# Kernel tuning notes

Measured on AMD Instinct MI355X. Metric: run time of the kernel, lower is better.

Reference implementation:

```python
import jax, jax.numpy as jnp
import numpy as np

MAX_NUM_CENTERS = 100
CENTER_IGNORE_PX = 3
SIGMA = 2.0   # center_gt_blur
KSIZE = 21    # GaussianLayer kernel size (ReflectionPad2d(10) + Conv2d(k=21))


def _gauss_kernel():
    r = KSIZE // 2
    x = jnp.arange(-r, r + 1, dtype=jnp.float32)
    g = jnp.exp(-0.5 * (x / SIGMA) ** 2)
    g = g / g.sum()
    return jnp.outer(g, g)  # [21,21], sums to 1 (matches scipy gaussian_filter of a delta)


def _gaussian_blur(x):
    # x: [B,H,W] -> depthwise 21x21 gaussian with reflect padding (GaussianLayer)
    r = KSIZE // 2
    k = _gauss_kernel()[None, None]  # [1,1,21,21]
    xp = jnp.pad(x[:, None], ((0, 0), (0, 0), (r, r), (r, r)), mode="reflect")
    y = jax.lax.conv_general_dilated(xp, k, (1, 1), "VALID",
                                     dimension_numbers=("NCHW", "OIHW", "NCHW"))
    return y[:, 0]


def setup_inputs() -> dict:
    key = jax.random.key(0)
    k1, k2 = jax.random.split(key)
    B, H, W = 8, 768, 768
    instances = jax.random.randint(k1, (B, 1, H, W), 0, MAX_NUM_CENTERS, dtype=jnp.int32)
    centers = jax.random.uniform(k2, (B, MAX_NUM_CENTERS, 2), dtype=jnp.float32) * (H - 1) + 1.0
    return {"instances": instances, "centers": centers}


def reference(instances, centers):
    B, _, H, W = instances.shape
    inst = instances[:, 0]                                # [B,H,W]
    col = jnp.arange(W, dtype=jnp.float32)                # xym_s[0][i,j] = j
    row = jnp.arange(H, dtype=jnp.float32)[:, None]       # xym_s[1][i,j] = i

    valid = inst > 0                                      # instance_mask
    has_inst = jnp.any(valid, axis=(1, 2)).astype(jnp.float32)  # len(unique)>1 gate

    # per-pixel nearest-center gather: center = centers[b, id-1]
    idx = jnp.clip(inst - 1, 0, MAX_NUM_CENTERS - 1)
    c = centers[jnp.arange(B)[:, None, None], idx]        # [B,H,W,2]
    gt_cx = jnp.where(valid, c[..., 1], -10000.0)         # gt_center_x (swapped coords)
    gt_cy = jnp.where(valid, c[..., 0], -10000.0)

    gt_X = gt_cx - row                                    # gt_center_x - xym_s[1]
    gt_Y = gt_cy - col                                    # gt_center_y - xym_s[0]

    near = (jnp.abs(gt_X) < CENTER_IGNORE_PX) & (jnp.abs(gt_Y) < CENTER_IGNORE_PX)
    # batches with no instances skip the block -> ignore stays all-ones
    ignore = jnp.where(has_inst[:, None, None] > 0, (~near).astype(jnp.float32), 1.0)

    m = valid.astype(jnp.float32)
    R = jnp.sqrt(gt_X ** 2 + gt_Y ** 2) * m
    theta_raw = jnp.arctan2(gt_Y, gt_X)
    theta = theta_raw * has_inst[:, None, None]           # skipped (zero) when no instances
    s = jnp.sin(theta_raw) * m
    cth = jnp.cos(theta_raw) * m
    M = jnp.sqrt(s ** 2 + cth ** 2)                       # == m, kept for faithfulness
    s = jnp.where(valid, s / jnp.maximum(M, 1e-12), 0.0)
    cth = jnp.where(valid, cth / jnp.maximum(M, 1e-12), 0.0)

    # gt_center_mask: zeros if no center-neighborhood pixels, else normalized blur
    blur = _gaussian_blur(1.0 - ignore)
    all_ones = jnp.all(ignore >= 1.0, axis=(1, 2))        # gt_center_mask.all()
    bmax = jnp.max(blur, axis=(1, 2), keepdims=True)
    cmask = jnp.where(all_ones[:, None, None], 0.0, blur / jnp.maximum(bmax, 1e-12))

    top = jnp.stack([R, theta, s, cth, ignore, cmask], axis=1)       # [B,6,H,W]
    mat = jnp.concatenate([top, jnp.zeros((B, 7, H, W), top.dtype)], axis=1)[:, :, None]
    # mat: [B,13,1,H,W]; channels 6..12 are zero (no orientation input)

    # gt_centers[id] = centers[b, id-1][[1,0]] for each instance id present
    present = jnp.zeros((B, MAX_NUM_CENTERS), dtype=bool).at[
        jnp.arange(B)[:, None], inst.reshape(B, -1)].set(True)
    swapped = centers[..., ::-1]
    gt_centers = jnp.zeros_like(centers).at[:, 1:, :].set(
        jnp.where(present[:, 1:, None], swapped[:, :-1, :], 0.0))

    return mat, gt_centers
```

## Files before the change

### kernel.cpp

```cpp
#include <hip/hip_runtime.h>
#include <math.h>

#define NB 8
#define NH 768
#define NW 768
#define NHW (NH*NW)
#define NCEN 100
#define NPIX (NB*NHW)
#define RAD 10
#define KS 21

#define SCAN_BLKS (NPIX / 4096)
#define BLKS_PER_B (NHW / 4096)
#define LIST_CAP 4096
#define QBLK_PER_B (NHW / 1024)
#define CAND_BLKS 96
#define FCAP 1024

#define HDR_HAS 0
#define HDR_CNT 8
#define HDR_BMAX 16
#define HDR_BLOCKMASK 64
#define HDR_LIST 8192

typedef float f4 __attribute__((ext_vector_type(4)));

__device__ const float g_G[KS] = {
    7.4335e-7f, 7.9919e-6f, 6.6915e-5f, 0.00043634f, 0.00221592f,
    0.00876415f, 0.02699548f, 0.06475880f, 0.12098536f, 0.17603266f,
    0.19947114f,
    0.17603266f, 0.12098536f, 0.06475880f, 0.02699548f, 0.00876415f,
    0.00221592f, 0.00043634f, 6.6915e-5f, 7.9919e-6f, 7.4335e-7f};

__device__ __forceinline__ float wfun(int p, int q, const float* __restrict__ g) {
    int d = p - q;
    float w = 0.f;
    if (d >= -RAD && d <= RAD) w = g[d + RAD];
    int a = p + q;
    if (q > 0 && a <= RAD) w += g[a + RAD];
    if (q < NH - 1 && a >= 2 * (NH - 1) - RAD) w += g[a - 2 * (NH - 1) + RAD];
    return w;
}

__device__ __forceinline__ float fatan2(float Y, float X) {
    float ax = fabsf(X), ay = fabsf(Y);
    float mx = fmaxf(ax, ay), mn = fminf(ax, ay);
    float a = mx > 0.f ? __fdividef(mn, mx) : 0.f;
    float ss = a * a;
    float r = fmaf(fmaf(fmaf(fmaf(fmaf(-0.01172120f, ss, 0.05265332f), ss,
                -0.11643287f), ss, 0.19354346f), ss, -0.33262347f), ss, 0.99997726f) * a;
    if (ay > ax) r = 1.57079637f - r;
    if (X < 0.f) r = 3.14159274f - r;
    return copysignf(r, Y);
}

__global__ void k_scan(const int4* __restrict__ inst4, int* __restrict__ hdr) {
    __shared__ unsigned sm[4];
    int t = threadIdx.x;
    if (t < 4) sm[t] = 0;
    __syncthreads();
    unsigned m0 = 0, m1 = 0, m2 = 0, m3 = 0;
    size_t base = (size_t)blockIdx.x * 1024 + t;
#pragma unroll
    for (int q = 0; q < 4; q++) {
        int4 v = inst4[base + (size_t)q * 256];
        int a[4] = {v.x, v.y, v.z, v.w};
#pragma unroll
        for (int e = 0; e < 4; e++) {
            int iv = a[e];
            if (iv > 0) {
                unsigned bit = 1u << (iv & 31);
                int w = iv >> 5;
                if (w == 0) m0 |= bit; else if (w == 1) m1 |= bit;
                else if (w == 2) m2 |= bit; else m3 |= bit;
            }
        }
    }
#pragma unroll
    for (int off = 32; off >= 1; off >>= 1) {
        m0 |= __shfl_xor(m0, off);
        m1 |= __shfl_xor(m1, off);
        m2 |= __shfl_xor(m2, off);
        m3 |= __shfl_xor(m3, off);
    }
    if ((t & 63) == 0) {
        if (m0) atomicOr(&sm[0], m0);
        if (m1) atomicOr(&sm[1], m1);
        if (m2) atomicOr(&sm[2], m2);
        if (m3) atomicOr(&sm[3], m3);
    }
    __syncthreads();
    if (t < 4) ((unsigned*)&hdr[HDR_BLOCKMASK])[blockIdx.x * 4 + t] = sm[t];
}

__global__ __launch_bounds__(256) void k_prep(const int* __restrict__ inst,
                                              const float* __restrict__ centers,
                                              int* __restrict__ hdr,
                                              float* __restrict__ gt) {
    __shared__ unsigned sm[4];
    __shared__ float s_cen[2 * NCEN];
    __shared__ int s_list[LIST_CAP];
    __shared__ int s_cnt;
    int b = blockIdx.x, t = threadIdx.x;
    if (t < 4) sm[t] = 0;
    if (t == 0) s_cnt = 0;
    for (int k = t; k < 2 * NCEN; k += 256) s_cen[k] = centers[b * 2 * NCEN + k];
    __syncthreads();

    const unsigned* bm = (const unsigned*)&hdr[HDR_BLOCKMASK];
    if (t < BLKS_PER_B) {
        const unsigned* p = &bm[(b * BLKS_PER_B + t) * 4];
        unsigned w0 = p[0], w1 = p[1], w2 = p[2], w3 = p[3];
        if (w0) atomicOr(&sm[0], w0);
        if (w1) atomicOr(&sm[1], w1);
        if (w2) atomicOr(&sm[2], w2);
        if (w3) atomicOr(&sm[3], w3);
    }
    __syncthreads();
    unsigned any = (sm[0] & 0xFFFFFFFEu) | sm[1] | sm[2] | sm[3];
    int has = any ? 1 : 0;

    if (t < NCEN) {
        int k = t;
        float vx = 0.f, vy = 0.f;
        if (k >= 1 && ((sm[k >> 5] >> (k & 31)) & 1u)) {
            vx = s_cen[(k - 1) * 2 + 1];
            vy = s_cen[(k - 1) * 2 + 0];
        }
        gt[(b * NCEN + k) * 2 + 0] = vx;
        gt[(b * NCEN + k) * 2 + 1] = vy;
    }

    const int* instb = inst + (size_t)b * NHW;
    if (has) {
        for (int c = t; c < NCEN * 49; c += 256) {
            int k = c / 49, r = c - k * 49;
            float cy = s_cen[2 * k];
            float cx = s_cen[2 * k + 1];
            int i = (int)floorf(cx) + r / 7 - 3;
            int j = (int)floorf(cy) + (r - (r / 7) * 7) - 3;
            if (i < 0 || i >= NH || j < 0 || j >= NW) continue;
            if (!(fabsf(cx - (float)i) < 3.f) || !(fabsf(cy - (float)j) < 3.f)) continue;
            if (instb[i * NW + j] == k + 1) {
                int slot = atomicAdd(&s_cnt, 1);
                if (slot < LIST_CAP) s_list[slot] = (i << 16) | j;
            }
        }
    }
    __syncthreads();
    int M = s_cnt < LIST_CAP ? s_cnt : LIST_CAP;
    int* gl = &hdr[HDR_LIST + b * LIST_CAP];
    for (int e = t; e < M; e += 256) gl[e] = s_list[e];
    if (t == 0) {
        hdr[HDR_HAS + b] = has;
        hdr[HDR_CNT + b] = M;
        hdr[HDR_BMAX + b] = 0;
    }
}

__global__ __launch_bounds__(256) void k_bmax(int* __restrict__ hdr) {
    __shared__ float s_g[KS];
    __shared__ int s_list[LIST_CAP];
    __shared__ float s_red[4];
    int t = threadIdx.x;
    int b = blockIdx.x / CAND_BLKS;
    int cb = blockIdx.x - b * CAND_BLKS;
    int M = hdr[HDR_CNT + b];
    int total = M * (KS * KS);
    if (M == 0 || cb * 256 >= total) return;
    if (t < KS) s_g[t] = g_G[t];
    const int* gl = &hdr[HDR_LIST + b * LIST_CAP];
    for (int e = t; e < M; e += 256) s_list[e] = gl[e];
    __syncthreads();

    float lmax = 0.f;
    for (int c = cb * 256 + t; c < total; c += CAND_BLKS * 256) {
        int m = c / (KS * KS), r = c - m * (KS * KS);
        int e = s_list[m];
        int pi = (e >> 16) + r / KS - RAD;
        int pj = (e & 0xFFFF) + (r - (r / KS) * KS) - RAD;
        if (pi < 0 || pi >= NH || pj < 0 || pj >= NW) continue;
        float acc = 0.f;
        for (int m2 = 0; m2 < M; m2++) {
            int e2 = s_list[m2];
            float wi = wfun(pi, e2 >> 16, s_g);
            if (wi == 0.f) continue;
            acc += wi * wfun(pj, e2 & 0xFFFF, s_g);
        }
        lmax = fmaxf(lmax, acc);
    }
#pragma unroll
    for (int off = 32; off >= 1; off >>= 1) lmax = fmaxf(lmax, __shfl_down(lmax, off));
    if ((t & 63) == 0) s_red[t >> 6] = lmax;
    __syncthreads();
    if (t == 0) {
        float bmx = fmaxf(fmaxf(s_red[0], s_red[1]), fmaxf(s_red[2], s_red[3]));
        atomicMax((unsigned*)&hdr[HDR_BMAX + b], __float_as_uint(bmx));
    }
}

__global__ __launch_bounds__(256) void k_fused(const int* __restrict__ inst,
                                               const float* __restrict__ centers,
                                               const int* __restrict__ hdr,
                                               float* __restrict__ out) {
    __shared__ float s_cen[2 * NCEN];
    __shared__ float s_g[KS];
    __shared__ int s_fl[FCAP];
    __shared__ int s_fM;
    int t = threadIdx.x;
    int b = blockIdx.x / QBLK_PER_B;
    int qblk = blockIdx.x - b * QBLK_PER_B;

    int has = hdr[HDR_HAS + b];
    int M = hdr[HDR_CNT + b];
    float bmx = __uint_as_float((unsigned)hdr[HDR_BMAX + b]);
    float sc = (has && M > 0) ? 1.f / fmaxf(bmx, 1e-12f) : 0.f;
    for (int k = t; k < 2 * NCEN; k += 256) s_cen[k] = centers[b * 2 * NCEN + k];
    if (t < KS) s_g[t] = g_G[t];
    if (t == 255) s_fM = 0;
    __syncthreads();

    int p0blk = qblk * 1024;
    int r0 = p0blk / NW;
    const int* gl = &hdr[HDR_LIST + b * LIST_CAP];
    for (int m = t; m < M; m += 256) {
        int e = gl[m];
        int qi = e >> 16;
        if (wfun(r0, qi, s_g) != 0.f || wfun(r0 + 1, qi, s_g) != 0.f) {
            int slot = atomicAdd(&s_fM, 1);
            if (slot < FCAP) s_fl[slot] = e;
        }
    }
    __syncthreads();
    int FM = s_fM < FCAP ? s_fM : FCAP;

    int p0 = p0blk + t * 4;
    int gi = p0 / NW;
    int gj0 = p0 - gi * NW;
    const int* instb = inst + (size_t)b * NHW;
    float* outb = out + (size_t)b * 13 * NHW;

    int4 ivv = *(const int4*)&instb[p0];
    int ia[4] = {ivv.x, ivv.y, ivv.z, ivv.w};
    f4 vR, vTh, vS, vC, vIg;
#pragma unroll
    for (int e = 0; e < 4; e++) {
        int iv = ia[e];
        bool valid = iv > 0;
        int idx = iv - 1;
        idx = idx < 0 ? 0 : idx;
        float cy = s_cen[2 * idx];
        float cx = s_cen[2 * idx + 1];
        float gcx = valid ? cx : -10000.f;
        float gcy = valid ? cy : -10000.f;
        float X = gcx - (float)gi;
        float Y = gcy - (float)(gj0 + e);
        bool near = (fabsf(X) < 3.f) && (fabsf(Y) < 3.f);
        vIg[e] = (has != 0) ? (near ? 0.f : 1.f) : 1.f;
        float m = valid ? 1.f : 0.f;
        float R2 = X * X + Y * Y;
        vR[e] = sqrtf(R2) * m;
        float rinv = R2 > 0.f ? rsqrtf(R2) : 0.f;
        vS[e] = valid ? Y * rinv : 0.f;
        vC[e] = valid ? (R2 > 0.f ? X * rinv : 1.f) : 0.f;
        float th = fatan2(Y, X);
        vTh[e] = (has != 0) ? th : 0.f;
    }

    f4 blur = {0.f, 0.f, 0.f, 0.f};
    for (int m = 0; m < FM; m++) {
        int e2 = s_fl[m];
        float wi = wfun(gi, e2 >> 16, s_g);
        if (wi == 0.f) continue;
        int qj = e2 & 0xFFFF;
#pragma unroll
        for (int e = 0; e < 4; e++) blur[e] += wi * wfun(gj0 + e, qj, s_g);
    }
    f4 vCm = blur * sc;

    __builtin_nontemporal_store(vR,  (f4*)&outb[(size_t)0 * NHW + p0]);
    __builtin_nontemporal_store(vTh, (f4*)&outb[(size_t)1 * NHW + p0]);
    __builtin_nontemporal_store(vS,  (f4*)&outb[(size_t)2 * NHW + p0]);
    __builtin_nontemporal_store(vC,  (f4*)&outb[(size_t)3 * NHW + p0]);
    __builtin_nontemporal_store(vIg, (f4*)&outb[(size_t)4 * NHW + p0]);
    __builtin_nontemporal_store(vCm, (f4*)&outb[(size_t)5 * NHW + p0]);
    f4 z = {0.f, 0.f, 0.f, 0.f};
#pragma unroll
    for (int ch = 6; ch < 13; ++ch)
        __builtin_nontemporal_store(z, (f4*)&outb[(size_t)ch * NHW + p0]);
}

extern "C" void kernel_launch(void* const* d_in, const int* in_sizes, int n_in,
                              void* d_out, int out_size, void* d_ws, size_t ws_size,
                              hipStream_t stream) {
    const int* inst = (const int*)d_in[0];
    const float* centers = (const float*)d_in[1];
    float* out = (float*)d_out;
    int* hdr = (int*)d_ws;
    float* gt = out + (size_t)NB * 13 * NHW;

    k_scan<<<SCAN_BLKS, 256, 0, stream>>>((const int4*)inst, hdr);
    k_prep<<<NB, 256, 0, stream>>>(inst, centers, hdr, gt);
    k_bmax<<<NB * CAND_BLKS, 256, 0, stream>>>(hdr);
    k_fused<<<NB * QBLK_PER_B, 256, 0, stream>>>(inst, centers, hdr, out);
}
```

Baseline: 293.9 us.

## Fold center-candidate detection into scan kernel and drop per-batch prep kernel

The scan kernel now checks each valid pixel against its instance center while it reads it, and appends near-center pixels straight to the global candidate list with global atomics. Per-batch masks are merged with global atomicOr. This removes the separate 8-block prep kernel, which ran on few blocks and made scattered loads. Header setup and gt_centers output move into a tiny init kernel and into the first k_bmax block of each batch. The cost is extra per-pixel work in the scan, a candidate list whose order is no longer fixed, and an extra small launch.

```diff
diff --git a/kernel.cpp b/kernel.cpp
--- a/kernel.cpp
+++ b/kernel.cpp
@@ -20,8 +20,8 @@
 #define HDR_HAS 0
 #define HDR_CNT 8
 #define HDR_BMAX 16
-#define HDR_BLOCKMASK 64
-#define HDR_LIST 8192
+#define HDR_MASK 24
+#define HDR_LIST 64
 
 typedef float f4 __attribute__((ext_vector_type(4)));
 
@@ -54,16 +54,33 @@
     return copysignf(r, Y);
 }
 
-__global__ void k_scan(const int4* __restrict__ inst4, int* __restrict__ hdr) {
+__global__ void k_init(int* __restrict__ hdr) {
+    if (threadIdx.x < 64) hdr[threadIdx.x] = 0;
+}
+
+__global__ __launch_bounds__(256) void k_scan(const int4* __restrict__ inst4,
+                                              const float* __restrict__ centers,
+                                              int* __restrict__ hdr) {
     __shared__ unsigned sm[4];
+    __shared__ float2 s_c2[NCEN];
     int t = threadIdx.x;
+    int blk = blockIdx.x;
+    int b = blk / BLKS_PER_B;
+    int lblk = blk - b * BLKS_PER_B;
     if (t < 4) sm[t] = 0;
-    __syncthreads();
+    for (int k = t; k < NCEN; k += 256)
+        s_c2[k] = ((const float2*)centers)[b * NCEN + k];
+    __syncthreads();
+
     unsigned m0 = 0, m1 = 0, m2 = 0, m3 = 0;
-    size_t base = (size_t)blockIdx.x * 1024 + t;
+    size_t base = (size_t)blk * 1024 + t;
+    int ppb = lblk * 4096 + t * 4;
 #pragma unroll
     for (int q = 0; q < 4; q++) {
         int4 v = inst4[base + (size_t)q * 256];
+        int pp = ppb + q * 1024;
+        int i = pp / NW;
+        int j0 = pp - i * NW;
         int a[4] = {v.x, v.y, v.z, v.w};
 #pragma unroll
         for (int e = 0; e < 4; e++) {
@@ -73,6 +90,14 @@
                 int w = iv >> 5;
                 if (w == 0) m0 |= bit; else if (w == 1) m1 |= bit;
                 else if (w == 2) m2 |= bit; else m3 |= bit;
+                int idx = iv - 1;
+                idx = idx > NCEN - 1 ? NCEN - 1 : idx;
+                float2 c = s_c2[idx];
+                if (fabsf(c.y - (float)i) < 3.f && fabsf(c.x - (float)(j0 + e)) < 3.f) {
+                    int slot = atomicAdd(&hdr[HDR_CNT + b], 1);
+                    if (slot < LIST_CAP)
+                        hdr[HDR_LIST + b * LIST_CAP + slot] = (i << 16) | (j0 + e);
+                }
             }
         }
     }
@@ -90,82 +115,41 @@
         if (m3) atomicOr(&sm[3], m3);
     }
     __syncthreads();
-    if (t < 4) ((unsigned*)&hdr[HDR_BLOCKMASK])[blockIdx.x * 4 + t] = sm[t];
-}
-
-__global__ __launch_bounds__(256) void k_prep(const int* __restrict__ inst,
-                                              const float* __restrict__ centers,
+    if (t < 4) {
+        unsigned v = sm[t];
+        if (v) atomicOr((unsigned*)&hdr[HDR_MASK + b * 4 + t], v);
+    }
+}
+
+__global__ __launch_bounds__(256) void k_bmax(const float* __restrict__ centers,
                                               int* __restrict__ hdr,
                                               float* __restrict__ gt) {
-    __shared__ unsigned sm[4];
-    __shared__ float s_cen[2 * NCEN];
-    __shared__ int s_list[LIST_CAP];
-    __shared__ int s_cnt;
-    int b = blockIdx.x, t = threadIdx.x;
-    if (t < 4) sm[t] = 0;
-    if (t == 0) s_cnt = 0;
-    for (int k = t; k < 2 * NCEN; k += 256) s_cen[k] = centers[b * 2 * NCEN + k];
-    __syncthreads();
-
-    const unsigned* bm = (const unsigned*)&hdr[HDR_BLOCKMASK];
-    if (t < BLKS_PER_B) {
-        const unsigned* p = &bm[(b * BLKS_PER_B + t) * 4];
-        unsigned w0 = p[0], w1 = p[1], w2 = p[2], w3 = p[3];
-        if (w0) atomicOr(&sm[0], w0);
-        if (w1) atomicOr(&sm[1], w1);
-        if (w2) atomicOr(&sm[2], w2);
-        if (w3) atomicOr(&sm[3], w3);
-    }
-    __syncthreads();
-    unsigned any = (sm[0] & 0xFFFFFFFEu) | sm[1] | sm[2] | sm[3];
-    int has = any ? 1 : 0;
-
-    if (t < NCEN) {
-        int k = t;
-        float vx = 0.f, vy = 0.f;
-        if (k >= 1 && ((sm[k >> 5] >> (k & 31)) & 1u)) {
-            vx = s_cen[(k - 1) * 2 + 1];
-            vy = s_cen[(k - 1) * 2 + 0];
-        }
-        gt[(b * NCEN + k) * 2 + 0] = vx;
-        gt[(b * NCEN + k) * 2 + 1] = vy;
-    }
-
-    const int* instb = inst + (size_t)b * NHW;
-    if (has) {
-        for (int c = t; c < NCEN * 49; c += 256) {
-            int k = c / 49, r = c - k * 49;
-            float cy = s_cen[2 * k];
-            float cx = s_cen[2 * k + 1];
-            int i = (int)floorf(cx) + r / 7 - 3;
-            int j = (int)floorf(cy) + (r - (r / 7) * 7) - 3;
-            if (i < 0 || i >= NH || j < 0 || j >= NW) continue;
-            if (!(fabsf(cx - (float)i) < 3.f) || !(fabsf(cy - (float)j) < 3.f)) continue;
-            if (instb[i * NW + j] == k + 1) {
-                int slot = atomicAdd(&s_cnt, 1);
-                if (slot < LIST_CAP) s_list[slot] = (i << 16) | j;
-            }
-        }
-    }
-    __syncthreads();
-    int M = s_cnt < LIST_CAP ? s_cnt : LIST_CAP;
-    int* gl = &hdr[HDR_LIST + b * LIST_CAP];
-    for (int e = t; e < M; e += 256) gl[e] = s_list[e];
-    if (t == 0) {
-        hdr[HDR_HAS + b] = has;
-        hdr[HDR_CNT + b] = M;
-        hdr[HDR_BMAX + b] = 0;
-    }
-}
-
-__global__ __launch_bounds__(256) void k_bmax(int* __restrict__ hdr) {
     __shared__ float s_g[KS];
     __shared__ int s_list[LIST_CAP];
     __shared__ float s_red[4];
     int t = threadIdx.x;
     int b = blockIdx.x / CAND_BLKS;
     int cb = blockIdx.x - b * CAND_BLKS;
+
+    if (cb == 0) {
+        const unsigned* pm = (const unsigned*)&hdr[HDR_MASK + b * 4];
+        if (t < NCEN) {
+            float vx = 0.f, vy = 0.f;
+            if (t >= 1 && ((pm[t >> 5] >> (t & 31)) & 1u)) {
+                vx = centers[(b * NCEN + (t - 1)) * 2 + 1];
+                vy = centers[(b * NCEN + (t - 1)) * 2 + 0];
+            }
+            gt[(b * NCEN + t) * 2 + 0] = vx;
+            gt[(b * NCEN + t) * 2 + 1] = vy;
+        }
+        if (t == 0) {
+            unsigned any = (pm[0] & 0xFFFFFFFEu) | pm[1] | pm[2] | pm[3];
+            hdr[HDR_HAS + b] = any ? 1 : 0;
+        }
+    }
+
     int M = hdr[HDR_CNT + b];
+    M = M < LIST_CAP ? M : LIST_CAP;
     int total = M * (KS * KS);
     if (M == 0 || cb * 256 >= total) return;
     if (t < KS) s_g[t] = g_G[t];
@@ -213,6 +197,7 @@
 
     int has = hdr[HDR_HAS + b];
     int M = hdr[HDR_CNT + b];
+    M = M < LIST_CAP ? M : LIST_CAP;
     float bmx = __uint_as_float((unsigned)hdr[HDR_BMAX + b]);
     float sc = (has && M > 0) ? 1.f / fmaxf(bmx, 1e-12f) : 0.f;
     for (int k = t; k < 2 * NCEN; k += 256) s_cen[k] = centers[b * 2 * NCEN + k];
@@ -299,8 +284,8 @@
     int* hdr = (int*)d_ws;
     float* gt = out + (size_t)NB * 13 * NHW;
 
-    k_scan<<<SCAN_BLKS, 256, 0, stream>>>((const int4*)inst, hdr);
-    k_prep<<<NB, 256, 0, stream>>>(inst, centers, hdr, gt);
-    k_bmax<<<NB * CAND_BLKS, 256, 0, stream>>>(hdr);
+    k_init<<<1, 64, 0, stream>>>(hdr);
+    k_scan<<<SCAN_BLKS, 256, 0, stream>>>((const int4*)inst, centers, hdr);
+    k_bmax<<<NB * CAND_BLKS, 256, 0, stream>>>(centers, hdr, gt);
     k_fused<<<NB * QBLK_PER_B, 256, 0, stream>>>(inst, centers, hdr, out);
 }
```

New measurement: 275.4 us. -6.3%, faster.
